# Performance work log

Hardware: AMD Instinct MI355X
Metric: run time of the kernel (lower is better)

## Reference

```python
import jax, jax.numpy as jnp
import numpy as np

D_MODEL = 2048
N_HEADS = 16
D_HEAD = 128
ROPE_THETA = 10000.0


def _rope(x, offset):
    # x: [B, H, S, D]; half-rotation RoPE with position offset
    B, H, S, D = x.shape
    inv_freq = 1.0 / (ROPE_THETA ** (jnp.arange(0, D, 2, dtype=jnp.float32) / D))  # [D/2]
    pos = (offset + jnp.arange(S, dtype=jnp.float32))                              # [S]
    ang = pos[:, None] * inv_freq[None, :]                                         # [S, D/2]
    cos = jnp.cos(ang).astype(x.dtype)
    sin = jnp.sin(ang).astype(x.dtype)
    x1, x2 = x[..., : D // 2], x[..., D // 2 :]
    return jnp.concatenate([x1 * cos - x2 * sin, x2 * cos + x1 * sin], axis=-1)


def setup_inputs() -> dict:
    key = jax.random.key(0)
    ks = jax.random.split(key, 5)
    B, Sq, Skv = 4, 1024, 1024
    x = jax.random.normal(ks[0], (B, Sq, D_MODEL), dtype=jnp.float32)
    cache_k = jax.random.normal(ks[1], (B, N_HEADS, Skv, D_HEAD), dtype=jnp.float32)
    cache_v = jax.random.normal(ks[2], (B, N_HEADS, Skv, D_HEAD), dtype=jnp.float32)
    w_qkv = jax.random.normal(ks[3], (D_MODEL, 3 * D_MODEL), dtype=jnp.float32) * (D_MODEL ** -0.5)
    w_o = jax.random.normal(ks[4], (D_MODEL, D_MODEL), dtype=jnp.float32) * (D_MODEL ** -0.5)
    return {"x": x, "cache_k": cache_k, "cache_v": cache_v, "w_qkv": w_qkv, "w_o": w_o}


def reference(x, cache_k, cache_v, w_qkv, w_o):
    B, S, _ = x.shape
    offset = cache_k.shape[2]
    # fused QKV projection: [B, S, 3*d_model] -> [B, H, S, 3*d_head]
    qkv = jnp.einsum("bsd,de->bse", x, w_qkv)
    qkv = qkv.reshape(B, S, N_HEADS, 3 * D_HEAD).transpose(0, 2, 1, 3)
    q, k, v = jnp.split(qkv, 3, axis=-1)
    q = _rope(q, offset)
    k = _rope(k, offset)
    # KV-cache concat along sequence dim
    k = jnp.concatenate([cache_k, k], axis=2)  # [B, H, Skv+S, D]
    v = jnp.concatenate([cache_v, v], axis=2)
    # SDPA (no mask, matching mask=None path)
    scale = D_HEAD ** -0.5
    scores = jnp.einsum("bhqd,bhkd->bhqk", q, k) * scale
    attn = jax.nn.softmax(scores, axis=-1)
    out = jnp.einsum("bhqk,bhkd->bhqd", attn, v)           # [B, H, S, D]
    out = out.transpose(0, 2, 1, 3).reshape(B, S, D_MODEL)
    return jnp.einsum("bsd,de->bse", out, w_o)
```

## Files before the change

kernel.cpp:

```cpp
#include <hip/hip_runtime.h>


typedef __bf16 bf16x8 __attribute__((ext_vector_type(8)));
typedef float f32x4 __attribute__((ext_vector_type(4)));
typedef unsigned short u16x8 __attribute__((ext_vector_type(8)));
typedef unsigned short u16x4 __attribute__((ext_vector_type(4)));

__device__ __forceinline__ float b2f(unsigned short u) {
  return __builtin_bit_cast(float, (unsigned int)u << 16);
}
__device__ __forceinline__ unsigned short f2b(float f) {
  unsigned int x = __builtin_bit_cast(unsigned int, f);
  x += 0x7fffu + ((x >> 16) & 1u);
  return (unsigned short)(x >> 16);
}
__device__ __forceinline__ unsigned int cvt_pk_bf16(float lo, float hi) {
  unsigned int r;
  asm("v_cvt_pk_bf16_f32 %0, %1, %2" : "=v"(r) : "v"(lo), "v"(hi));
  return r;
}
__device__ __forceinline__ void gload_lds16(const void* g, void* l) {
  __builtin_amdgcn_global_load_lds(
      (__attribute__((address_space(1))) void*)(g),
      (__attribute__((address_space(3))) void*)(l), 16, 0, 0);
}
__device__ __forceinline__ void barrier_nodrain() {
  asm volatile("" ::: "memory");
  __builtin_amdgcn_s_barrier();
  asm volatile("" ::: "memory");
}

__global__ void build_trig(float* __restrict__ cs, float* __restrict__ sn) {
  int idx = blockIdx.x * 256 + threadIdx.x;
  int s = idx >> 6, i = idx & 63;
  float inv = exp2f(-(float)i * (13.287712379549449f / 64.0f));
  float ang = (float)(1024 + s) * inv;
  cs[idx] = cosf(ang);
  sn[idx] = sinf(ang);
}

__global__ void conv_bf16(const float* __restrict__ in, unsigned short* __restrict__ out) {
  size_t i = ((size_t)blockIdx.x * 256 + threadIdx.x) * 8;
  float4 a = *(const float4*)(in + i);
  float4 b = *(const float4*)(in + i + 4);
  u16x8 v;
  v[0] = f2b(a.x); v[1] = f2b(a.y); v[2] = f2b(a.z); v[3] = f2b(a.w);
  v[4] = f2b(b.x); v[5] = f2b(b.y); v[6] = f2b(b.z); v[7] = f2b(b.w);
  *(u16x8*)(out + i) = v;
}

__global__ __launch_bounds__(256) void transpose_conv(
    const float* __restrict__ in, unsigned short* __restrict__ out, int R, int C) {
  __shared__ float tile[32][33];
  int c0 = blockIdx.x * 32, r0 = blockIdx.y * 32;
  int tx = threadIdx.x & 31, ty = threadIdx.x >> 5;
#pragma unroll
  for (int j = 0; j < 4; ++j)
    tile[ty + j * 8][tx] = in[(size_t)(r0 + ty + j * 8) * C + c0 + tx];
  __syncthreads();
#pragma unroll
  for (int j = 0; j < 4; ++j)
    out[(size_t)(c0 + ty + j * 8) * R + r0 + tx] = f2b(tile[tx][ty + j * 8]);
}

__global__ void copy_k(const float* __restrict__ ck, unsigned short* __restrict__ Kf) {
  size_t idx = ((size_t)blockIdx.x * 256 + threadIdx.x) * 4;
  size_t bh = idx >> 17, rem = idx & 131071;
  float4 a = *(const float4*)(ck + idx);
  u16x4 v;
  v[0] = f2b(a.x); v[1] = f2b(a.y); v[2] = f2b(a.z); v[3] = f2b(a.w);
  *(u16x4*)(Kf + bh * 262144 + rem) = v;
}

__global__ __launch_bounds__(256) void rope_qk(
    const unsigned short* __restrict__ qkv, const float* __restrict__ cs,
    const float* __restrict__ sn, unsigned short* __restrict__ Qb,
    unsigned short* __restrict__ Kf) {
  int row = blockIdx.x;
  int b = row >> 10, s = row & 1023;
#pragma unroll
  for (int it = 0; it < 4; ++it) {
    int item = it * 256 + threadIdx.x;
    int h = item >> 6, i = item & 63;
    const unsigned short* base = qkv + (size_t)row * 6144 + h * 384;
    float q1 = b2f(base[i]),       q2 = b2f(base[64 + i]);
    float k1 = b2f(base[128 + i]), k2 = b2f(base[192 + i]);
    float c = cs[s * 64 + i], sv = sn[s * 64 + i];
    const float scale = 0.12751738f;
    size_t bh = (size_t)(b * 16 + h);
    unsigned short* qd = Qb + (bh * 1024 + s) * 128;
    qd[i]      = f2b((q1 * c - q2 * sv) * scale);
    qd[64 + i] = f2b((q2 * c + q1 * sv) * scale);
    unsigned short* kd = Kf + (bh * 2048 + 1024 + s) * 128;
    kd[i]      = f2b(k1 * c - k2 * sv);
    kd[64 + i] = f2b(k2 * c + k1 * sv);
  }
}

__global__ __launch_bounds__(256) void build_vt(
    const float* __restrict__ cv, const unsigned short* __restrict__ qkv,
    unsigned short* __restrict__ Vt) {
  __shared__ float tile[32][33];
  int bhid = blockIdx.z;
  int s0 = blockIdx.x * 32, d0 = blockIdx.y * 32;
  int tx = threadIdx.x & 31, ty = threadIdx.x >> 5;
  int b = bhid >> 4, h = bhid & 15;
#pragma unroll
  for (int j = 0; j < 4; ++j) {
    int s = s0 + ty + j * 8, d = d0 + tx;
    float v;
    if (s < 1024) v = cv[((size_t)bhid * 1024 + s) * 128 + d];
    else v = b2f(qkv[((size_t)b * 1024 + (s - 1024)) * 6144 + h * 384 + 256 + d]);
    tile[ty + j * 8][tx] = v;
  }
  __syncthreads();
#pragma unroll
  for (int j = 0; j < 4; ++j) {
    int d = d0 + ty + j * 8, s = s0 + tx;
    Vt[((size_t)bhid * 128 + d) * 2048 + s] = f2b(tile[tx][ty + j * 8]);
  }
}

template <int M, int N, int K, bool OUT_BF16>
__global__ __launch_bounds__(512, 4) void gemm_ring(
    const unsigned short* __restrict__ A, const unsigned short* __restrict__ B,
    void* __restrict__ Cout) {
  __shared__ __align__(16) char lds[3 * 24576];
  constexpr int NT = N / 128;
  constexpr int Kt = K / 32;
  int bid = blockIdx.x;
  int tm = bid / NT, tn = bid % NT;
  int tid = threadIdx.x;
  int lane = tid & 63, wave = tid >> 6;
  int wr = (wave >> 1) * 64, wc = (wave & 1) * 64;
  int l15 = lane & 15, g = lane >> 4;

  int p = tid * 16;
  const unsigned short* aSrc0 = A + (size_t)(tm * 256 + (p >> 6)) * K + ((p & 63) >> 1);
  const unsigned short* aSrc1 = aSrc0 + (size_t)128 * K;
  const unsigned short* bSrc  = B + (size_t)(tn * 128 + (p >> 6)) * K + ((p & 63) >> 1);

  f32x4 acc[4][4] = {};

  auto stage = [&](int s) {
    char* base = (char*)lds + s * 24576;
    gload_lds16(aSrc0, base + p);
    gload_lds16(aSrc1, base + 8192 + p);
    gload_lds16(bSrc,  base + 16384 + p);
    aSrc0 += 32; aSrc1 += 32; bSrc += 32;
  };

  stage(0);
  stage(1);
  asm volatile("s_waitcnt vmcnt(3)" ::: "memory");

  int slot = 0, sNext = 2;
  for (int t = 0; t < Kt; ++t) {
    barrier_nodrain();
    if (t + 2 < Kt) {
      stage(sNext);
      sNext = (sNext == 2) ? 0 : sNext + 1;
      asm volatile("s_waitcnt vmcnt(3)" ::: "memory");
    } else {
      asm volatile("s_waitcnt vmcnt(0)" ::: "memory");
    }
    const char* As_ = (const char*)lds + slot * 24576;
    const char* Bs_ = As_ + 16384;
    bf16x8 af[4], bfr[4];
#pragma unroll
    for (int m = 0; m < 4; ++m)
      af[m] = *(const bf16x8*)(As_ + (wr + m * 16 + l15) * 64 + g * 16);
#pragma unroll
    for (int n = 0; n < 4; ++n)
      bfr[n] = *(const bf16x8*)(Bs_ + (wc + n * 16 + l15) * 64 + g * 16);
    __builtin_amdgcn_s_setprio(1);
#pragma unroll
    for (int m = 0; m < 4; ++m)
#pragma unroll
      for (int n = 0; n < 4; ++n)
        acc[m][n] = __builtin_amdgcn_mfma_f32_16x16x32_bf16(af[m], bfr[n], acc[m][n], 0, 0, 0);
    __builtin_amdgcn_s_setprio(0);
    slot = (slot == 2) ? 0 : slot + 1;
  }

#pragma unroll
  for (int m = 0; m < 4; ++m) {
    int row0 = tm * 256 + wr + m * 16 + g * 4;
#pragma unroll
    for (int n = 0; n < 4; ++n) {
      int col = tn * 128 + wc + n * 16 + l15;
#pragma unroll
      for (int r = 0; r < 4; ++r) {
        size_t off = (size_t)(row0 + r) * N + col;
        if constexpr (OUT_BF16) ((unsigned short*)Cout)[off] = f2b(acc[m][n][r]);
        else ((float*)Cout)[off] = acc[m][n][r];
      }
    }
  }
}

__global__ __launch_bounds__(256, 2) void attn_kernel(
    const unsigned short* __restrict__ Qb,
    const unsigned short* __restrict__ Kf,
    const unsigned short* __restrict__ Vt,
    unsigned short* __restrict__ Out) {
  __shared__ __align__(16) unsigned short Ks[2][64 * 128];
  __shared__ __align__(16) unsigned short Vs[2][64 * 128];
  __shared__ __align__(16) char PsRaw[4 * 2 * 2048];

  int raw = blockIdx.x;
  int sb = (raw & 7) * 64 + (raw >> 3);
  int bh = sb >> 3, qt = sb & 7;
  int tid = threadIdx.x, lane = tid & 63, wave = tid >> 6;
  int l15 = lane & 15, g = lane >> 4;
  int swz = (l15 & 7) << 4;

  int qrow0 = qt * 128 + wave * 32;
  bf16x8 qf0[4], qf1[4];
  const unsigned short* qp0 = Qb + ((size_t)(bh * 1024 + qrow0 + l15)) * 128;
#pragma unroll
  for (int kk = 0; kk < 4; ++kk) {
    qf0[kk] = *(const bf16x8*)(qp0 + kk * 32 + g * 8);
    qf1[kk] = *(const bf16x8*)(qp0 + 16 * 128 + kk * 32 + g * 8);
  }

  u16x8 ou;
#pragma unroll
  for (int j = 0; j < 8; ++j) ou[j] = 0x3F80;
  bf16x8 ones = __builtin_bit_cast(bf16x8, ou);

  const unsigned short* Kbase = Kf + (size_t)bh * 2048 * 128;
  const unsigned short* Vbase = Vt + (size_t)bh * 128 * 2048;
  const unsigned short* kptr[4];
  const unsigned short* vptr[4];
  char* kdst0[4];
  char* vdst0[4];
#pragma unroll
  for (int is = 0; is < 4; ++is) {
    int p = tid * 16 + is * 4096;
    int lgk = p ^ (((p >> 8) & 7) << 4);
    kptr[is] = Kbase + (size_t)(lgk >> 8) * 128 + ((lgk & 255) >> 1);
    kdst0[is] = (char*)Ks + is * 4096 + (tid & 192) * 16;
    int lgv = p ^ (((p >> 7) & 7) << 4);
    vptr[is] = Vbase + (size_t)(lgv >> 7) * 2048 + ((lgv & 127) >> 1);
    vdst0[is] = (char*)Vs + is * 4096 + (tid & 192) * 16;
  }
  char* ps0 = PsRaw + wave * 4096 + l15 * 128;
  char* ps1 = ps0 + 2048;

  auto stage = [&](int buf) {
#pragma unroll
    for (int is = 0; is < 4; ++is) {
      gload_lds16(kptr[is], kdst0[is] + buf * 16384);  kptr[is] += 64 * 128;
      gload_lds16(vptr[is], vdst0[is] + buf * 16384);  vptr[is] += 64;
    }
  };

  float mrun0 = -1e30f, mrun1 = -1e30f;
  f32x4 acc0[8] = {}, acc1[8] = {};
  f32x4 accl0 = {}, accl1 = {};

  auto softmax_pack = [&](f32x4* st, float& mrun, f32x4* accp, f32x4& accl,
                          char* ps) {
    float m0 = fmaxf(fmaxf(st[0][0], st[0][1]), st[0][2]);
    float m1 = fmaxf(fmaxf(st[0][3], st[1][0]), st[1][1]);
    float m2 = fmaxf(fmaxf(st[1][2], st[1][3]), st[2][0]);
    float m3 = fmaxf(fmaxf(st[2][1], st[2][2]), st[2][3]);
    float m4 = fmaxf(fmaxf(st[3][0], st[3][1]), st[3][2]);
    float pmax = fmaxf(fmaxf(fmaxf(m0, m1), fmaxf(m2, m3)), fmaxf(m4, st[3][3]));
    pmax = fmaxf(pmax, __shfl_xor(pmax, 16));
    pmax = fmaxf(pmax, __shfl_xor(pmax, 32));
    if (!__all(pmax - mrun <= 8.0f)) {
      float mnew = fmaxf(mrun, pmax);
      float corr = exp2f(mrun - mnew);
      accl *= corr;
#pragma unroll
      for (int mt = 0; mt < 8; ++mt) accp[mt] *= corr;
      mrun = mnew;
    }
#pragma unroll
    for (int t = 0; t < 4; ++t) {
      float p0 = exp2f(st[t][0] - mrun);
      float p1 = exp2f(st[t][1] - mrun);
      float p2 = exp2f(st[t][2] - mrun);
      float p3 = exp2f(st[t][3] - mrun);
      uint2 w;
      w.x = cvt_pk_bf16(p0, p1);
      w.y = cvt_pk_bf16(p2, p3);
      *(uint2*)(ps + ((t * 32 + g * 8) ^ swz)) = w;
    }
  };

  stage(0);
  for (int it = 0; it < 32; ++it) {
    int cur = it & 1;
    barrier_nodrain();
    if (it + 1 < 32) {
      stage(cur ^ 1);
      asm volatile("s_waitcnt vmcnt(8)" ::: "memory");
    } else {
      asm volatile("s_waitcnt vmcnt(0)" ::: "memory");
    }
    barrier_nodrain();
    const char* ksA = (const char*)Ks + cur * 16384 + l15 * 256;
    const char* vsA = (const char*)Vs + cur * 16384 + l15 * 128;

    f32x4 st0[4] = {}, st1[4] = {};
#pragma unroll
    for (int kk = 0; kk < 4; ++kk) {
#pragma unroll
      for (int t = 0; t < 4; ++t) {
        bf16x8 a = *(const bf16x8*)(ksA + t * 4096 + ((kk * 64 + g * 16) ^ swz));
        st0[t] = __builtin_amdgcn_mfma_f32_16x16x32_bf16(a, qf0[kk], st0[t], 0, 0, 0);
        st1[t] = __builtin_amdgcn_mfma_f32_16x16x32_bf16(a, qf1[kk], st1[t], 0, 0, 0);
      }
    }

    softmax_pack(st0, mrun0, acc0, accl0, ps0);
    softmax_pack(st1, mrun1, acc1, accl1, ps1);

#pragma unroll
    for (int k2 = 0; k2 < 2; ++k2) {
      bf16x8 p0 = *(const bf16x8*)(ps0 + ((k2 * 64 + g * 16) ^ swz));
      bf16x8 p1 = *(const bf16x8*)(ps1 + ((k2 * 64 + g * 16) ^ swz));
      accl0 = __builtin_amdgcn_mfma_f32_16x16x32_bf16(ones, p0, accl0, 0, 0, 0);
      accl1 = __builtin_amdgcn_mfma_f32_16x16x32_bf16(ones, p1, accl1, 0, 0, 0);
#pragma unroll
      for (int mt = 0; mt < 8; ++mt) {
        bf16x8 a = *(const bf16x8*)(vsA + mt * 2048 + ((k2 * 64 + g * 16) ^ swz));
        acc0[mt] = __builtin_amdgcn_mfma_f32_16x16x32_bf16(a, p0, acc0[mt], 0, 0, 0);
        acc1[mt] = __builtin_amdgcn_mfma_f32_16x16x32_bf16(a, p1, acc1[mt], 0, 0, 0);
      }
    }
  }

  float inv0 = 1.f / accl0[0];
  float inv1 = 1.f / accl1[0];
  int b = bh >> 4, h = bh & 15;
  int sq = qt * 128 + wave * 32 + l15;
  unsigned short* orow0 = Out + ((size_t)(b * 1024 + sq) * 16 + h) * 128;
  unsigned short* orow1 = orow0 + (size_t)16 * 2048;
#pragma unroll
  for (int mt = 0; mt < 8; ++mt) {
    uint2 w0, w1;
    w0.x = cvt_pk_bf16(acc0[mt][0] * inv0, acc0[mt][1] * inv0);
    w0.y = cvt_pk_bf16(acc0[mt][2] * inv0, acc0[mt][3] * inv0);
    w1.x = cvt_pk_bf16(acc1[mt][0] * inv1, acc1[mt][1] * inv1);
    w1.y = cvt_pk_bf16(acc1[mt][2] * inv1, acc1[mt][3] * inv1);
    *(uint2*)(orow0 + mt * 16 + g * 4) = w0;
    *(uint2*)(orow1 + mt * 16 + g * 4) = w1;
  }
}

extern "C" void kernel_launch(void* const* d_in, const int* in_sizes, int n_in,
                              void* d_out, int out_size, void* d_ws, size_t ws_size,
                              hipStream_t stream) {
  const float* x       = (const float*)d_in[0];
  const float* cache_k = (const float*)d_in[1];
  const float* cache_v = (const float*)d_in[2];
  const float* w_qkv   = (const float*)d_in[3];
  const float* w_o     = (const float*)d_in[4];
  float* out = (float*)d_out;

  char* W = (char*)d_ws;
  constexpr size_t O_TRIG = 0;
  constexpr size_t O_XB   = 524288;
  constexpr size_t O_WQT  = O_XB  + 16777216;
  constexpr size_t O_WOT  = O_WQT + 25165824;
  constexpr size_t O_QKV  = O_WOT + 8388608;
  constexpr size_t O_QB   = O_QKV + 50331648;
  constexpr size_t O_KF   = O_QB  + 16777216;
  constexpr size_t O_VT   = O_KF  + 33554432;
  float* cs_tab = (float*)(W + O_TRIG);
  float* sn_tab = (float*)(W + O_TRIG + 262144);
  unsigned short* xb   = (unsigned short*)(W + O_XB);
  unsigned short* wqT  = (unsigned short*)(W + O_WQT);
  unsigned short* woT  = (unsigned short*)(W + O_WOT);
  unsigned short* qkv  = (unsigned short*)(W + O_QKV);
  unsigned short* qb   = (unsigned short*)(W + O_QB);
  unsigned short* Kf   = (unsigned short*)(W + O_KF);
  unsigned short* Vt   = (unsigned short*)(W + O_VT);
  unsigned short* attn_out = xb;

  build_trig<<<256, 256, 0, stream>>>(cs_tab, sn_tab);
  conv_bf16<<<4096, 256, 0, stream>>>(x, xb);
  transpose_conv<<<dim3(192, 64), 256, 0, stream>>>(w_qkv, wqT, 2048, 6144);
  transpose_conv<<<dim3(64, 64), 256, 0, stream>>>(w_o, woT, 2048, 2048);
  gemm_ring<4096, 6144, 2048, true><<<768, 512, 0, stream>>>(xb, wqT, qkv);
  rope_qk<<<4096, 256, 0, stream>>>(qkv, cs_tab, sn_tab, qb, Kf);
  copy_k<<<8192, 256, 0, stream>>>(cache_k, Kf);
  build_vt<<<dim3(64, 4, 64), 256, 0, stream>>>(cache_v, qkv, Vt);
  attn_kernel<<<512, 256, 0, stream>>>(qb, Kf, Vt, attn_out);
  gemm_ring<4096, 2048, 2048, false><<<256, 512, 0, stream>>>(attn_out, woT, out);
}
```

Baseline: 335.7 us.

## Double K tile to 64 with XOR-swizzled LDS and double buffering in GEMM

The bf16 GEMM now loads 64-wide K slices per stage instead of 32, replacing the 3-slot ring with a 2-slot double buffer. LDS rows are XOR-swizzled on both the global-to-LDS store and the fragment reads to avoid bank conflicts from the wider 128-byte rows. Fewer barriers per unit of K and more MFMA work per stage are intended to cut synchronisation overhead. In exchange, LDS per block doubles, occupancy drops (launch bounds 4 to 2), and an extra barrier is added per iteration.

```diff
diff --git a/kernel.cpp b/kernel.cpp
--- a/kernel.cpp
+++ b/kernel.cpp
@@ -122,65 +122,83 @@
 }
 
 template <int M, int N, int K, bool OUT_BF16>
-__global__ __launch_bounds__(512, 4) void gemm_ring(
+__global__ __launch_bounds__(512, 2) void gemm_ring(
     const unsigned short* __restrict__ A, const unsigned short* __restrict__ B,
     void* __restrict__ Cout) {
-  __shared__ __align__(16) char lds[3 * 24576];
+  __shared__ __align__(16) char lds[2 * 49152];
   constexpr int NT = N / 128;
-  constexpr int Kt = K / 32;
+  constexpr int Kt = K / 64;
   int bid = blockIdx.x;
   int tm = bid / NT, tn = bid % NT;
   int tid = threadIdx.x;
   int lane = tid & 63, wave = tid >> 6;
   int wr = (wave >> 1) * 64, wc = (wave & 1) * 64;
   int l15 = lane & 15, g = lane >> 4;
-
-  int p = tid * 16;
-  const unsigned short* aSrc0 = A + (size_t)(tm * 256 + (p >> 6)) * K + ((p & 63) >> 1);
-  const unsigned short* aSrc1 = aSrc0 + (size_t)128 * K;
-  const unsigned short* bSrc  = B + (size_t)(tn * 128 + (p >> 6)) * K + ((p & 63) >> 1);
+  int swz = (l15 & 7) << 4;
+
+  const unsigned short* aS[4];
+  const unsigned short* bS[2];
+#pragma unroll
+  for (int i = 0; i < 4; ++i) {
+    int p = tid * 16 + i * 8192;
+    int row = p >> 7, c = (p & 127) ^ ((row & 7) << 4);
+    aS[i] = A + (size_t)(tm * 256 + row) * K + (c >> 1);
+  }
+#pragma unroll
+  for (int i = 0; i < 2; ++i) {
+    int p = tid * 16 + i * 8192;
+    int row = p >> 7, c = (p & 127) ^ ((row & 7) << 4);
+    bS[i] = B + (size_t)(tn * 128 + row) * K + (c >> 1);
+  }
 
   f32x4 acc[4][4] = {};
 
   auto stage = [&](int s) {
-    char* base = (char*)lds + s * 24576;
-    gload_lds16(aSrc0, base + p);
-    gload_lds16(aSrc1, base + 8192 + p);
-    gload_lds16(bSrc,  base + 16384 + p);
-    aSrc0 += 32; aSrc1 += 32; bSrc += 32;
+    char* base = (char*)lds + s * 49152;
+#pragma unroll
+    for (int i = 0; i < 4; ++i) {
+      gload_lds16(aS[i], base + tid * 16 + i * 8192);
+      aS[i] += 64;
+    }
+#pragma unroll
+    for (int i = 0; i < 2; ++i) {
+      gload_lds16(bS[i], base + 32768 + tid * 16 + i * 8192);
+      bS[i] += 64;
+    }
   };
 
   stage(0);
-  stage(1);
-  asm volatile("s_waitcnt vmcnt(3)" ::: "memory");
-
-  int slot = 0, sNext = 2;
   for (int t = 0; t < Kt; ++t) {
+    int cur = t & 1;
     barrier_nodrain();
-    if (t + 2 < Kt) {
-      stage(sNext);
-      sNext = (sNext == 2) ? 0 : sNext + 1;
-      asm volatile("s_waitcnt vmcnt(3)" ::: "memory");
+    if (t + 1 < Kt) {
+      stage(cur ^ 1);
+      asm volatile("s_waitcnt vmcnt(6)" ::: "memory");
     } else {
       asm volatile("s_waitcnt vmcnt(0)" ::: "memory");
     }
-    const char* As_ = (const char*)lds + slot * 24576;
-    const char* Bs_ = As_ + 16384;
-    bf16x8 af[4], bfr[4];
-#pragma unroll
-    for (int m = 0; m < 4; ++m)
-      af[m] = *(const bf16x8*)(As_ + (wr + m * 16 + l15) * 64 + g * 16);
-#pragma unroll
-    for (int n = 0; n < 4; ++n)
-      bfr[n] = *(const bf16x8*)(Bs_ + (wc + n * 16 + l15) * 64 + g * 16);
-    __builtin_amdgcn_s_setprio(1);
-#pragma unroll
-    for (int m = 0; m < 4; ++m)
+    barrier_nodrain();
+    const char* As_ = (const char*)lds + cur * 49152;
+    const char* Bs_ = As_ + 32768;
+#pragma unroll
+    for (int h = 0; h < 2; ++h) {
+      bf16x8 af[4], bfr[4];
+#pragma unroll
+      for (int m = 0; m < 4; ++m)
+        af[m] = *(const bf16x8*)(As_ + (wr + m * 16 + l15) * 128 +
+                                 ((h * 64 + g * 16) ^ swz));
 #pragma unroll
       for (int n = 0; n < 4; ++n)
-        acc[m][n] = __builtin_amdgcn_mfma_f32_16x16x32_bf16(af[m], bfr[n], acc[m][n], 0, 0, 0);
-    __builtin_amdgcn_s_setprio(0);
-    slot = (slot == 2) ? 0 : slot + 1;
+        bfr[n] = *(const bf16x8*)(Bs_ + (wc + n * 16 + l15) * 128 +
+                                  ((h * 64 + g * 16) ^ swz));
+      __builtin_amdgcn_s_setprio(1);
+#pragma unroll
+      for (int m = 0; m < 4; ++m)
+#pragma unroll
+        for (int n = 0; n < 4; ++n)
+          acc[m][n] = __builtin_amdgcn_mfma_f32_16x16x32_bf16(af[m], bfr[n], acc[m][n], 0, 0, 0);
+      __builtin_amdgcn_s_setprio(0);
+    }
   }
 
 #pragma unroll
```

New measurement: 333.0 us. No clear change (-0.8%).
